# Kernel optimization log

Hardware: AMD Instinct MI355X
Metric: run time of the kernel (lower is better)

The kernel has to match this reference:

```python
import jax, jax.numpy as jnp
import numpy as np

B, S, D_MODEL, N_HEADS = 2, 2048, 1024, 16
HEAD_DIM = D_MODEL // N_HEADS
BASE = 10000.0

# 3D RoPE slice sizes: n_pairs = head_dim//2 split into x,y,z
_n_pairs = HEAD_DIM // 2
_px = _n_pairs // 3
_py = _n_pairs // 3
_pz = _n_pairs - _px - _py
D_X, D_Y, D_Z = _px * 2, _py * 2, _pz * 2  # 20, 20, 24


def _rotate_half(x):
    # interleaved pairs: (x0,x1,x2,x3,...) -> (-x1,x0,-x3,x2,...)
    x1 = x[..., ::2]
    x2 = x[..., 1::2]
    return jnp.stack((-x2, x1), axis=-1).reshape(x.shape)


def _rope_apply(x, pos, dim):
    # x: [B,H,S,dim]; pos: [B,S] int coords
    if dim == 0:
        return x
    inv_freq = 1.0 / (BASE ** (jnp.arange(0, dim, 2, dtype=jnp.float32) / dim))
    t = pos.astype(jnp.float32)[..., None] * inv_freq          # [B,S,dim//2]
    cos = jnp.repeat(jnp.cos(t), 2, axis=-1)[:, None]          # [B,1,S,dim]
    sin = jnp.repeat(jnp.sin(t), 2, axis=-1)[:, None]
    return x * cos + _rotate_half(x) * sin


def _rope3d(q, k, pos_xyz):
    s1, s2, s3 = D_X, D_X + D_Y, D_X + D_Y + D_Z
    parts_q, parts_k = [], []
    for (a, b), ax in (((0, s1), 0), ((s1, s2), 1), ((s2, s3), 2)):
        d = b - a
        parts_q.append(_rope_apply(q[..., a:b], pos_xyz[..., ax], d))
        parts_k.append(_rope_apply(k[..., a:b], pos_xyz[..., ax], d))
    return jnp.concatenate(parts_q, axis=-1), jnp.concatenate(parts_k, axis=-1)


def setup_inputs() -> dict:
    key = jax.random.key(0)
    k1, k2, k3, k4 = jax.random.split(key, 4)
    hidden_states = jax.random.normal(k1, (B, S, D_MODEL), dtype=jnp.float32)
    # padding: each batch row keeps first `len` tokens
    lengths = jnp.array([S - 37, S - 130], dtype=jnp.int32)
    attention_mask = jnp.arange(S)[None, :] < lengths[:, None]          # [B,S] bool, True=keep
    causal_mask = jnp.triu(jnp.ones((S, S), dtype=bool), k=1)[None, None]  # True=masked
    pos_xyz = jax.random.randint(k2, (B, S, 3), 0, 30).astype(jnp.int32)
    w_qkv = jax.random.normal(k3, (3 * D_MODEL, D_MODEL), dtype=jnp.float32) * (D_MODEL ** -0.5)
    w_out = jax.random.normal(k4, (D_MODEL, D_MODEL), dtype=jnp.float32) * (D_MODEL ** -0.5)
    return {"hidden_states": hidden_states, "w_qkv": w_qkv, "w_out": w_out,
            "attention_mask": attention_mask, "causal_mask": causal_mask,
            "pos_xyz": pos_xyz}


def reference(hidden_states, w_qkv, w_out, attention_mask, causal_mask, pos_xyz):
    Bb, Ss, Dd = hidden_states.shape
    scale = HEAD_DIM ** -0.5
    qkv = jnp.einsum('bsd,ed->bse', hidden_states, w_qkv)               # [B,S,3D]
    qkv = qkv.reshape(Bb, Ss, 3, N_HEADS, HEAD_DIM).transpose(2, 0, 3, 1, 4)
    q, k, v = qkv[0], qkv[1], qkv[2]                                    # [B,H,S,hd]
    q, k = _rope3d(q, k, pos_xyz)
    scores = jnp.einsum('bhqd,bhkd->bhqk', q, k) * scale                # [B,H,S,S]
    scores = jnp.where(causal_mask, -jnp.inf, scores)
    scores = jnp.where(attention_mask[:, None, None, :], scores, -jnp.inf)
    weights = jax.nn.softmax(scores, axis=-1)                           # dropout p=0 (eval)
    out = jnp.einsum('bhqk,bhkd->bhqd', weights, v)
    out = out.transpose(0, 2, 1, 3).reshape(Bb, Ss, Dd)
    return jnp.einsum('bsd,ed->bse', out, w_out)
```

## Files before the change

kernel.cpp:

```cpp
#include <hip/hip_runtime.h>
#include <math.h>

extern "C" __device__ float __ocml_native_exp2_f32(float);

namespace {

typedef __attribute__((ext_vector_type(8))) short short8;
typedef __attribute__((ext_vector_type(4))) short short4b;
typedef __attribute__((ext_vector_type(4))) float floatx4;

constexpr int B_ = 2;
constexpr int S_ = 2048;
constexpr int DM_ = 1024;
constexpr int NH_ = 16;
constexpr int HD_ = 64;

__device__ inline unsigned short f2bf(float f) {
  unsigned u = __builtin_bit_cast(unsigned, f);
  u += 0x7fffu + ((u >> 16) & 1u);
  return (unsigned short)(u >> 16);
}

template <int CTRL>
__device__ inline float dpp_ror(float x) {
  const int r = __builtin_amdgcn_update_dpp(
      0, __builtin_bit_cast(int, x), CTRL, 0xF, 0xF, false);
  return __builtin_bit_cast(float, r);
}

__device__ inline void gl2lds16(const unsigned short* g, unsigned short* l) {
  __builtin_amdgcn_global_load_lds(
      (const __attribute__((address_space(1))) unsigned int*)g,
      (__attribute__((address_space(3))) unsigned int*)l, 16, 0, 0);
}

__global__ __launch_bounds__(256) void prep(
    const float* __restrict__ hidden, const float* __restrict__ wqkv,
    const float* __restrict__ wout, const unsigned char* __restrict__ mask,
    unsigned short* __restrict__ hb, int* __restrict__ lengths) {
  const int bid = blockIdx.x;
  if (bid < 4096) {
    const int i = bid * 256 + threadIdx.x;
    const float* src;
    int off;
    if (i < 524288)              { src = hidden; off = 0; }
    else if (i < 524288 + 393216){ src = wqkv;   off = 524288; }
    else                         { src = wout;   off = 524288 + 393216; }
    const size_t j = (size_t)(i - off);
    const float4 a = ((const float4*)src)[j * 2];
    const float4 b = ((const float4*)src)[j * 2 + 1];
    short8 v;
    v[0] = (short)f2bf(a.x); v[1] = (short)f2bf(a.y);
    v[2] = (short)f2bf(a.z); v[3] = (short)f2bf(a.w);
    v[4] = (short)f2bf(b.x); v[5] = (short)f2bf(b.y);
    v[6] = (short)f2bf(b.z); v[7] = (short)f2bf(b.w);
    ((short8*)hb)[i] = v;
  } else {
    const int b = bid - 4096;
    const int es1 = (mask[1] != 0);
    __shared__ int cnt;
    if (threadIdx.x == 0) cnt = 0;
    __syncthreads();
    int local = 0;
    for (int s = threadIdx.x; s < S_; s += blockDim.x) {
      bool nz;
      if (es1) nz = mask[b * S_ + s] != 0;
      else     nz = ((const unsigned int*)mask)[b * S_ + s] != 0;
      local += nz ? 1 : 0;
    }
    atomicAdd(&cnt, local);
    __syncthreads();
    if (threadIdx.x == 0) lengths[b] = cnt;
  }
}

__global__ __launch_bounds__(256) void qkv_gemm(
    const unsigned short* __restrict__ A, const unsigned short* __restrict__ W,
    const int* __restrict__ pos_xyz,
    unsigned short* __restrict__ Qb, unsigned short* __restrict__ Kb,
    unsigned short* __restrict__ Vtb) {
  __shared__ __align__(16) unsigned short As[128 * 32];
  __shared__ __align__(16) unsigned short Bs[128 * 32];
  const int lin = blockIdx.y * gridDim.x + blockIdx.x;
  const int xcd = lin & 7, t = lin >> 3;
  const int mg = xcd >> 1, ng = xcd & 1;
  const int m0 = (mg * 8 + t / 12) * 128;
  const int n0 = (ng * 12 + t % 12) * 128;
  const int w = threadIdx.x >> 6, lane = threadIdx.x & 63;
  const int lm = lane & 15, q4 = lane >> 4;
  const int srow = w * 32;
  const int r_in = lane >> 2, c_in = (lane & 3) * 8;
  const int wr = (w >> 1) * 64, wc = (w & 1) * 64;
  const int which = n0 >> 10;
  floatx4 acc[4][4];
  const floatx4 z4 = {0.f, 0.f, 0.f, 0.f};
#pragma unroll
  for (int i = 0; i < 4; i++)
#pragma unroll
    for (int j = 0; j < 4; j++) acc[i][j] = z4;

  for (int k0 = 0; k0 < DM_; k0 += 32) {
    gl2lds16(A + (size_t)(m0 + srow + r_in) * DM_ + k0 + c_in, As + srow * 32);
    gl2lds16(A + (size_t)(m0 + srow + 16 + r_in) * DM_ + k0 + c_in,
             As + (srow + 16) * 32);
    gl2lds16(W + (size_t)(n0 + srow + r_in) * DM_ + k0 + c_in, Bs + srow * 32);
    gl2lds16(W + (size_t)(n0 + srow + 16 + r_in) * DM_ + k0 + c_in,
             Bs + (srow + 16) * 32);
    __syncthreads();
    short8 af[4], bf[4];
#pragma unroll
    for (int t2 = 0; t2 < 4; t2++)
      af[t2] = *(const short8*)(As + (wr + t2 * 16 + lm) * 32 + q4 * 8);
#pragma unroll
    for (int t2 = 0; t2 < 4; t2++)
      bf[t2] = *(const short8*)(Bs + (wc + t2 * 16 + lm) * 32 + q4 * 8);
    if (which == 2) {
#pragma unroll
      for (int i = 0; i < 4; i++)
#pragma unroll
        for (int j = 0; j < 4; j++)
          acc[i][j] = __builtin_amdgcn_mfma_f32_16x16x32_bf16(af[i], bf[j],
                                                              acc[i][j], 0, 0, 0);
    } else {
#pragma unroll
      for (int i = 0; i < 4; i++)
#pragma unroll
        for (int j = 0; j < 4; j++)
          acc[i][j] = __builtin_amdgcn_mfma_f32_16x16x32_bf16(bf[i], af[j],
                                                              acc[i][j], 0, 0, 0);
    }
    __syncthreads();
  }

  const int h = ((n0 + wc) & 1023) >> 6;
  if (which == 2) {
#pragma unroll
    for (int nt = 0; nt < 4; nt++) {
      const int d = nt * 16 + lm;
#pragma unroll
      for (int mt = 0; mt < 4; mt++) {
        const int m = m0 + wr + mt * 16 + q4 * 4;
        const int bi = m >> 11, si = m & (S_ - 1);
        short4b pk;
#pragma unroll
        for (int r = 0; r < 4; r++) pk[r] = (short)f2bf(acc[mt][nt][r]);
        *(short4b*)(Vtb + ((size_t)(bi * NH_ + h) * HD_ + d) * S_ + si) = pk;
      }
    }
  } else {
    unsigned short* Dst = (which == 0) ? Qb : Kb;
    const float osc = (which == 0) ? 0.125f * 1.44269504088896f : 1.0f;
#pragma unroll
    for (int nt = 0; nt < 4; nt++) {
      const int dbase = nt * 16 + q4 * 4;
      const int p0 = dbase >> 1;
      int axis, j0, dseg;
      if (p0 < 10)      { axis = 0; j0 = p0;      dseg = 20; }
      else if (p0 < 20) { axis = 1; j0 = p0 - 10; dseg = 20; }
      else              { axis = 2; j0 = p0 - 20; dseg = 24; }
      const float invf0 =
          __expf(-(2.0f * (float)j0 / (float)dseg) * 9.210340371976184f);
      const float invf1 =
          __expf(-(2.0f * (float)(j0 + 1) / (float)dseg) * 9.210340371976184f);
#pragma unroll
      for (int mt = 0; mt < 4; mt++) {
        const int m = m0 + wr + mt * 16 + lm;
        const int bi = m >> 11, si = m & (S_ - 1);
        const int pos = pos_xyz[((size_t)bi * S_ + si) * 3 + axis];
        short4b pk;
#pragma unroll
        for (int u = 0; u < 2; u++) {
          const float ve = acc[nt][mt][2 * u], vo = acc[nt][mt][2 * u + 1];
          float sn, cs;
          sincosf((float)pos * (u ? invf1 : invf0), &sn, &cs);
          pk[2 * u]     = (short)f2bf(fmaf(ve, cs, -vo * sn) * osc);
          pk[2 * u + 1] = (short)f2bf(fmaf(vo, cs, ve * sn) * osc);
        }
        *(short4b*)(Dst + ((size_t)(bi * NH_ + h) * S_ + si) * HD_ + dbase) = pk;
      }
    }
  }
}

__global__ __launch_bounds__(256) void flash_mfma(
    const unsigned short* __restrict__ Q, const unsigned short* __restrict__ Kg,
    const unsigned short* __restrict__ Vt, const int* __restrict__ lengths,
    unsigned short* __restrict__ Oa) {
  __shared__ __align__(16) unsigned short Ks[2 * 64 * 64];
  __shared__ __align__(16) unsigned short Vs[2 * 64 * 64];
  __shared__ __align__(16) unsigned short Ps[4][16 * 64];

  const int lin = blockIdx.y * gridDim.x + blockIdx.x;
  const int xcd = lin & 7, k = lin >> 3;
  const int s = k >> 5, c = k & 31;
  const int pc = (c & 1) ? 31 - (c >> 1) : (c >> 1);
  const int qt = (s & 1) ? 31 - pc : pc;
  const int bh = xcd * 4 + s;
  const int b = bh >> 4, h = bh & 15;
  const int q0 = qt * 64;

  const int w = threadIdx.x >> 6, lane = threadIdx.x & 63;
  const int lm = lane & 15, q4 = lane >> 4;
  const int len = lengths[b];
  const unsigned short* Qp = Q + (size_t)bh * S_ * HD_;
  const unsigned short* Kp = Kg + (size_t)bh * S_ * HD_;
  const unsigned short* Vp = Vt + (size_t)bh * HD_ * S_;

  const int r8 = lane >> 3, c8 = lane & 7;
  const int rs0 = w * 16 + r8, rs1 = rs0 + 8;
  const int cs = (c8 ^ (rs0 & 7)) << 3;
  const unsigned short* gK0 = Kp + (size_t)rs0 * HD_ + cs;
  const unsigned short* gK1 = Kp + (size_t)rs1 * HD_ + cs;
  const unsigned short* gV0 = Vp + (size_t)rs0 * S_ + cs;
  const unsigned short* gV1 = Vp + (size_t)rs1 * S_ + cs;
  unsigned short* dK0 = Ks + w * 16 * 64;
  unsigned short* dK1 = Ks + (w * 16 + 8) * 64;
  unsigned short* dV0 = Vs + w * 16 * 64;
  unsigned short* dV1 = Vs + (w * 16 + 8) * 64;

  const int qrow = q0 + w * 16 + lm;
  short8 qf[2];
  qf[0] = *(const short8*)(Qp + (size_t)qrow * HD_ + q4 * 8);
  qf[1] = *(const short8*)(Qp + (size_t)qrow * HD_ + 32 + q4 * 8);

  const floatx4 z4 = {0.f, 0.f, 0.f, 0.f};
  floatx4 o[4];
#pragma unroll
  for (int dt = 0; dt < 4; dt++) o[dt] = z4;
  float m_i[4], l_i[4];
#pragma unroll
  for (int r = 0; r < 4; r++) { m_i[r] = -1e30f; l_i[r] = 0.0f; }

  unsigned short* ps = Ps[w];
  const int ktiles = min(qt + 1, (len + 63) >> 6);

  gl2lds16(gK0, dK0);
  gl2lds16(gK1, dK1);
  gl2lds16(gV0, dV0);
  gl2lds16(gV1, dV1);
  __syncthreads();

  int cur = 0;
  for (int kt = 0; kt < ktiles; kt++) {
    const int k0 = kt * 64;
    if (kt + 1 < ktiles) {
      const size_t koff = (size_t)(k0 + 64) * HD_;
      const int nb = (cur ^ 1) * 4096;
      gl2lds16(gK0 + koff, dK0 + nb);
      gl2lds16(gK1 + koff, dK1 + nb);
      gl2lds16(gV0 + (k0 + 64), dV0 + nb);
      gl2lds16(gV1 + (k0 + 64), dV1 + nb);
    }
    const unsigned short* kc = Ks + cur * 4096;
    const unsigned short* vc = Vs + cur * 4096;

    floatx4 sc[4];
    __builtin_amdgcn_s_setprio(1);
#pragma unroll
    for (int nt = 0; nt < 4; nt++) {
      const int row = nt * 16 + lm, sw = row & 7;
      const unsigned short* kb = kc + row * 64;
      const short8 b0 = *(const short8*)(kb + ((q4 ^ sw) << 3));
      const short8 b1 = *(const short8*)(kb + (((q4 + 4) ^ sw) << 3));
      sc[nt] = __builtin_amdgcn_mfma_f32_16x16x32_bf16(qf[0], b0, z4, 0, 0, 0);
      sc[nt] = __builtin_amdgcn_mfma_f32_16x16x32_bf16(qf[1], b1, sc[nt], 0, 0, 0);
    }
    __builtin_amdgcn_s_setprio(0);
    if (kt == qt || k0 + 64 > len) {
#pragma unroll
      for (int nt = 0; nt < 4; nt++) {
        const int col = k0 + nt * 16 + lm;
#pragma unroll
        for (int r = 0; r < 4; r++) {
          const int row = q0 + w * 16 + q4 * 4 + r;
          if (col > row || col >= len) sc[nt][r] = -1e30f;
        }
      }
    }
    float mx[4];
#pragma unroll
    for (int r = 0; r < 4; r++) {
      float m0 = fmaxf(fmaxf(sc[0][r], sc[1][r]), fmaxf(sc[2][r], sc[3][r]));
      m0 = fmaxf(m0, dpp_ror<0x121>(m0));
      m0 = fmaxf(m0, dpp_ror<0x122>(m0));
      m0 = fmaxf(m0, dpp_ror<0x124>(m0));
      m0 = fmaxf(m0, dpp_ror<0x128>(m0));
      mx[r] = m0;
    }
    const bool ok = (mx[0] <= m_i[0] + 8.f) && (mx[1] <= m_i[1] + 8.f) &&
                    (mx[2] <= m_i[2] + 8.f) && (mx[3] <= m_i[3] + 8.f);
    if (!__all(ok)) {
#pragma unroll
      for (int r = 0; r < 4; r++) {
        const float mt = fmaxf(m_i[r], mx[r]);
        const float al = __ocml_native_exp2_f32(m_i[r] - mt);
        l_i[r] *= al;
        m_i[r] = mt;
#pragma unroll
        for (int dt = 0; dt < 4; dt++) o[dt][r] *= al;
      }
    }
#pragma unroll
    for (int r = 0; r < 4; r++) {
      float rs = 0.0f;
#pragma unroll
      for (int nt = 0; nt < 4; nt++) {
        const float pp = __ocml_native_exp2_f32(sc[nt][r] - m_i[r]);
        sc[nt][r] = pp;
        rs += pp;
      }
      rs += dpp_ror<0x121>(rs);
      rs += dpp_ror<0x122>(rs);
      rs += dpp_ror<0x124>(rs);
      rs += dpp_ror<0x128>(rs);
      l_i[r] += rs;
    }
#pragma unroll
    for (int nt = 0; nt < 4; nt++)
#pragma unroll
      for (int r = 0; r < 4; r++) {
        const int row = q4 * 4 + r;
        const int cc = (((nt * 2 + (lm >> 3)) ^ (row & 7)) << 3) | (lm & 7);
        ps[row * 64 + cc] = f2bf(sc[nt][r]);
      }
    __builtin_amdgcn_s_setprio(1);
#pragma unroll
    for (int ks = 0; ks < 2; ks++) {
      const short8 pf = *(const short8*)(
          ps + lm * 64 + ((((ks << 2) + q4) ^ (lm & 7)) << 3));
#pragma unroll
      for (int dt = 0; dt < 4; dt++) {
        const int row = dt * 16 + lm, sw = row & 7;
        const short8 vf = *(const short8*)(
            vc + row * 64 + ((((ks << 2) + q4) ^ sw) << 3));
        o[dt] = __builtin_amdgcn_mfma_f32_16x16x32_bf16(pf, vf, o[dt], 0, 0, 0);
      }
    }
    __builtin_amdgcn_s_setprio(0);
    __syncthreads();
    cur ^= 1;
  }
  float invl[4];
#pragma unroll
  for (int r = 0; r < 4; r++) invl[r] = 1.0f / l_i[r];
#pragma unroll
  for (int dt = 0; dt < 4; dt++)
#pragma unroll
    for (int r = 0; r < 4; r++) {
      const int row = q0 + w * 16 + q4 * 4 + r;
      const int col = h * HD_ + dt * 16 + lm;
      Oa[((size_t)b * S_ + row) * DM_ + col] = f2bf(o[dt][r] * invl[r]);
    }
}

__global__ __launch_bounds__(256) void out_gemm(
    const unsigned short* __restrict__ A, const unsigned short* __restrict__ W,
    float* __restrict__ C) {
  __shared__ __align__(16) unsigned short As[128 * 32];
  __shared__ __align__(16) unsigned short Bs[128 * 32];
  const int m0 = blockIdx.y * 128, n0 = blockIdx.x * 128;
  const int w = threadIdx.x >> 6, lane = threadIdx.x & 63;
  const int lm = lane & 15, q4 = lane >> 4;
  const int srow = w * 32;
  const int r_in = lane >> 2, c_in = (lane & 3) * 8;
  const int wr = (w >> 1) * 64, wc = (w & 1) * 64;
  floatx4 acc[4][4];
  const floatx4 z4 = {0.f, 0.f, 0.f, 0.f};
#pragma unroll
  for (int i = 0; i < 4; i++)
#pragma unroll
    for (int j = 0; j < 4; j++) acc[i][j] = z4;

  for (int k0 = 0; k0 < DM_; k0 += 32) {
    gl2lds16(A + (size_t)(m0 + srow + r_in) * DM_ + k0 + c_in, As + srow * 32);
    gl2lds16(A + (size_t)(m0 + srow + 16 + r_in) * DM_ + k0 + c_in,
             As + (srow + 16) * 32);
    gl2lds16(W + (size_t)(n0 + srow + r_in) * DM_ + k0 + c_in, Bs + srow * 32);
    gl2lds16(W + (size_t)(n0 + srow + 16 + r_in) * DM_ + k0 + c_in,
             Bs + (srow + 16) * 32);
    __syncthreads();
    short8 af[4], bf[4];
#pragma unroll
    for (int t = 0; t < 4; t++)
      af[t] = *(const short8*)(As + (wr + t * 16 + lm) * 32 + q4 * 8);
#pragma unroll
    for (int t = 0; t < 4; t++)
      bf[t] = *(const short8*)(Bs + (wc + t * 16 + lm) * 32 + q4 * 8);
#pragma unroll
    for (int i = 0; i < 4; i++)
#pragma unroll
      for (int j = 0; j < 4; j++)
        acc[i][j] =
            __builtin_amdgcn_mfma_f32_16x16x32_bf16(bf[i], af[j], acc[i][j],
                                                    0, 0, 0);
    __syncthreads();
  }
#pragma unroll
  for (int nt = 0; nt < 4; nt++) {
    const int nbase = n0 + wc + nt * 16 + q4 * 4;
#pragma unroll
    for (int mt = 0; mt < 4; mt++) {
      const int m = m0 + wr + mt * 16 + lm;
      *(floatx4*)(C + (size_t)m * DM_ + nbase) = acc[nt][mt];
    }
  }
}

}

extern "C" void kernel_launch(void* const* d_in, const int* in_sizes, int n_in,
                              void* d_out, int out_size, void* d_ws, size_t ws_size,
                              hipStream_t stream) {
  const float* hidden = (const float*)d_in[0];
  const float* w_qkv = (const float*)d_in[1];
  const float* w_out = (const float*)d_in[2];
  const unsigned char* amask = (const unsigned char*)d_in[3];
  const int* pos_xyz = (const int*)d_in[5];
  float* out = (float*)d_out;

  constexpr size_t NHID = (size_t)B_ * S_ * DM_;
  constexpr size_t NWQ = (size_t)3 * DM_ * DM_;
  constexpr size_t NWO = (size_t)DM_ * DM_;
  constexpr size_t NQKV = (size_t)B_ * NH_ * S_ * HD_;

  unsigned short* hb = (unsigned short*)d_ws;
  unsigned short* wqb = hb + NHID;
  unsigned short* wob = wqb + NWQ;
  unsigned short* Qb = wob + NWO;
  unsigned short* Kb = Qb + NQKV;
  unsigned short* Vtb = Kb + NQKV;
  unsigned short* attn = Vtb + NQKV;
  int* lens = (int*)(attn + NQKV);

  prep<<<dim3(4096 + B_), dim3(256), 0, stream>>>(hidden, w_qkv, w_out, amask,
                                                  hb, lens);
  qkv_gemm<<<dim3(3 * DM_ / 128, B_ * S_ / 128), dim3(256), 0, stream>>>(
      hb, wqb, pos_xyz, Qb, Kb, Vtb);
  flash_mfma<<<dim3(S_ / 64, B_ * NH_), dim3(256), 0, stream>>>(
      Qb, Kb, Vtb, lens, attn);
  out_gemm<<<dim3(DM_ / 128, B_ * S_ / 128), dim3(256), 0, stream>>>(
      attn, wob, out);
}
```

Before: 238.5 us.

## Deepen QKV GEMM K-step and shrink out-GEMM tiles with XCD-aware mapping

The QKV GEMM now stages two 32-wide K slices per barrier pair into doubled LDS buffers, halving the number of syncthreads per K sweep. The output GEMM switches from 128x128 to 64x64 tiles, giving 1024 blocks instead of 256 so all CUs are busy, and adds an XCD-aware block-to-tile remap. Smaller out-GEMM tiles lower per-block data reuse and raise global/L2 traffic, while the doubled QKV LDS footprint may cut occupancy.

```diff
diff --git a/kernel.cpp b/kernel.cpp
--- a/kernel.cpp
+++ b/kernel.cpp
@@ -79,8 +79,8 @@
     const int* __restrict__ pos_xyz,
     unsigned short* __restrict__ Qb, unsigned short* __restrict__ Kb,
     unsigned short* __restrict__ Vtb) {
-  __shared__ __align__(16) unsigned short As[128 * 32];
-  __shared__ __align__(16) unsigned short Bs[128 * 32];
+  __shared__ __align__(16) unsigned short As[2][128 * 32];
+  __shared__ __align__(16) unsigned short Bs[2][128 * 32];
   const int lin = blockIdx.y * gridDim.x + blockIdx.x;
   const int xcd = lin & 7, t = lin >> 3;
   const int mg = xcd >> 1, ng = xcd & 1;
@@ -99,35 +99,45 @@
 #pragma unroll
     for (int j = 0; j < 4; j++) acc[i][j] = z4;
 
-  for (int k0 = 0; k0 < DM_; k0 += 32) {
-    gl2lds16(A + (size_t)(m0 + srow + r_in) * DM_ + k0 + c_in, As + srow * 32);
-    gl2lds16(A + (size_t)(m0 + srow + 16 + r_in) * DM_ + k0 + c_in,
-             As + (srow + 16) * 32);
-    gl2lds16(W + (size_t)(n0 + srow + r_in) * DM_ + k0 + c_in, Bs + srow * 32);
-    gl2lds16(W + (size_t)(n0 + srow + 16 + r_in) * DM_ + k0 + c_in,
-             Bs + (srow + 16) * 32);
-    __syncthreads();
-    short8 af[4], bf[4];
-#pragma unroll
-    for (int t2 = 0; t2 < 4; t2++)
-      af[t2] = *(const short8*)(As + (wr + t2 * 16 + lm) * 32 + q4 * 8);
-#pragma unroll
-    for (int t2 = 0; t2 < 4; t2++)
-      bf[t2] = *(const short8*)(Bs + (wc + t2 * 16 + lm) * 32 + q4 * 8);
-    if (which == 2) {
-#pragma unroll
-      for (int i = 0; i < 4; i++)
-#pragma unroll
-        for (int j = 0; j < 4; j++)
-          acc[i][j] = __builtin_amdgcn_mfma_f32_16x16x32_bf16(af[i], bf[j],
-                                                              acc[i][j], 0, 0, 0);
-    } else {
-#pragma unroll
-      for (int i = 0; i < 4; i++)
-#pragma unroll
-        for (int j = 0; j < 4; j++)
-          acc[i][j] = __builtin_amdgcn_mfma_f32_16x16x32_bf16(bf[i], af[j],
-                                                              acc[i][j], 0, 0, 0);
+  const unsigned short* gA0 = A + (size_t)(m0 + srow + r_in) * DM_ + c_in;
+  const unsigned short* gA1 = A + (size_t)(m0 + srow + 16 + r_in) * DM_ + c_in;
+  const unsigned short* gB0 = W + (size_t)(n0 + srow + r_in) * DM_ + c_in;
+  const unsigned short* gB1 = W + (size_t)(n0 + srow + 16 + r_in) * DM_ + c_in;
+
+  for (int k0 = 0; k0 < DM_; k0 += 64) {
+#pragma unroll
+    for (int hh = 0; hh < 2; hh++) {
+      const int ko = k0 + hh * 32;
+      gl2lds16(gA0 + ko, As[hh] + srow * 32);
+      gl2lds16(gA1 + ko, As[hh] + (srow + 16) * 32);
+      gl2lds16(gB0 + ko, Bs[hh] + srow * 32);
+      gl2lds16(gB1 + ko, Bs[hh] + (srow + 16) * 32);
+    }
+    __syncthreads();
+#pragma unroll
+    for (int hh = 0; hh < 2; hh++) {
+      short8 af[4], bf[4];
+#pragma unroll
+      for (int t2 = 0; t2 < 4; t2++)
+        af[t2] = *(const short8*)(As[hh] + (wr + t2 * 16 + lm) * 32 + q4 * 8);
+#pragma unroll
+      for (int t2 = 0; t2 < 4; t2++)
+        bf[t2] = *(const short8*)(Bs[hh] + (wc + t2 * 16 + lm) * 32 + q4 * 8);
+      if (which == 2) {
+#pragma unroll
+        for (int i = 0; i < 4; i++)
+#pragma unroll
+          for (int j = 0; j < 4; j++)
+            acc[i][j] = __builtin_amdgcn_mfma_f32_16x16x32_bf16(
+                af[i], bf[j], acc[i][j], 0, 0, 0);
+      } else {
+#pragma unroll
+        for (int i = 0; i < 4; i++)
+#pragma unroll
+          for (int j = 0; j < 4; j++)
+            acc[i][j] = __builtin_amdgcn_mfma_f32_16x16x32_bf16(
+                bf[i], af[j], acc[i][j], 0, 0, 0);
+      }
     }
     __syncthreads();
   }
@@ -356,50 +366,49 @@
 __global__ __launch_bounds__(256) void out_gemm(
     const unsigned short* __restrict__ A, const unsigned short* __restrict__ W,
     float* __restrict__ C) {
-  __shared__ __align__(16) unsigned short As[128 * 32];
-  __shared__ __align__(16) unsigned short Bs[128 * 32];
-  const int m0 = blockIdx.y * 128, n0 = blockIdx.x * 128;
+  __shared__ __align__(16) unsigned short As[64 * 32];
+  __shared__ __align__(16) unsigned short Bs[64 * 32];
+  const int lin = blockIdx.y * gridDim.x + blockIdx.x;
+  const int xcd = lin & 7, t = lin >> 3;
+  const int m0 = (xcd * 8 + (t >> 4)) * 64;
+  const int n0 = (t & 15) * 64;
   const int w = threadIdx.x >> 6, lane = threadIdx.x & 63;
   const int lm = lane & 15, q4 = lane >> 4;
-  const int srow = w * 32;
+  const int srow = w * 16;
   const int r_in = lane >> 2, c_in = (lane & 3) * 8;
-  const int wr = (w >> 1) * 64, wc = (w & 1) * 64;
-  floatx4 acc[4][4];
+  const int wr = (w >> 1) * 32, wc = (w & 1) * 32;
+  floatx4 acc[2][2];
   const floatx4 z4 = {0.f, 0.f, 0.f, 0.f};
 #pragma unroll
-  for (int i = 0; i < 4; i++)
-#pragma unroll
-    for (int j = 0; j < 4; j++) acc[i][j] = z4;
+  for (int i = 0; i < 2; i++)
+#pragma unroll
+    for (int j = 0; j < 2; j++) acc[i][j] = z4;
 
   for (int k0 = 0; k0 < DM_; k0 += 32) {
     gl2lds16(A + (size_t)(m0 + srow + r_in) * DM_ + k0 + c_in, As + srow * 32);
-    gl2lds16(A + (size_t)(m0 + srow + 16 + r_in) * DM_ + k0 + c_in,
-             As + (srow + 16) * 32);
     gl2lds16(W + (size_t)(n0 + srow + r_in) * DM_ + k0 + c_in, Bs + srow * 32);
-    gl2lds16(W + (size_t)(n0 + srow + 16 + r_in) * DM_ + k0 + c_in,
-             Bs + (srow + 16) * 32);
-    __syncthreads();
-    short8 af[4], bf[4];
-#pragma unroll
-    for (int t = 0; t < 4; t++)
-      af[t] = *(const short8*)(As + (wr + t * 16 + lm) * 32 + q4 * 8);
-#pragma unroll
-    for (int t = 0; t < 4; t++)
-      bf[t] = *(const short8*)(Bs + (wc + t * 16 + lm) * 32 + q4 * 8);
-#pragma unroll
-    for (int i = 0; i < 4; i++)
-#pragma unroll
-      for (int j = 0; j < 4; j++)
+    __syncthreads();
+    short8 af[2], bf[2];
+#pragma unroll
+    for (int t2 = 0; t2 < 2; t2++)
+      af[t2] = *(const short8*)(As + (wr + t2 * 16 + lm) * 32 + q4 * 8);
+#pragma unroll
+    for (int t2 = 0; t2 < 2; t2++)
+      bf[t2] = *(const short8*)(Bs + (wc + t2 * 16 + lm) * 32 + q4 * 8);
+#pragma unroll
+    for (int i = 0; i < 2; i++)
+#pragma unroll
+      for (int j = 0; j < 2; j++)
         acc[i][j] =
             __builtin_amdgcn_mfma_f32_16x16x32_bf16(bf[i], af[j], acc[i][j],
                                                     0, 0, 0);
     __syncthreads();
   }
 #pragma unroll
-  for (int nt = 0; nt < 4; nt++) {
+  for (int nt = 0; nt < 2; nt++) {
     const int nbase = n0 + wc + nt * 16 + q4 * 4;
 #pragma unroll
-    for (int mt = 0; mt < 4; mt++) {
+    for (int mt = 0; mt < 2; mt++) {
       const int m = m0 + wr + mt * 16 + lm;
       *(floatx4*)(C + (size_t)m * DM_ + nbase) = acc[nt][mt];
     }
@@ -438,6 +447,5 @@
       hb, wqb, pos_xyz, Qb, Kb, Vtb);
   flash_mfma<<<dim3(S_ / 64, B_ * NH_), dim3(256), 0, stream>>>(
       Qb, Kb, Vtb, lens, attn);
-  out_gemm<<<dim3(DM_ / 128, B_ * S_ / 128), dim3(256), 0, stream>>>(
-      attn, wob, out);
-}
+  out_gemm<<<dim3(16, 64), dim3(256), 0, stream>>>(attn, wob, out);
+}
```

Measured after the change: 225.9 us. 5.3% less time.
